# Performance work log

Hardware: AMD Instinct MI355X
Metric: run time of the kernel (lower is better)

## Reference

```python
import jax, jax.numpy as jnp
import numpy as np

B, D_IN, D_EXP, D_TOW, N_EXP, N_TASK = 16384, 1024, 1024, 512, 8, 4


def setup_inputs() -> dict:
    key = jax.random.key(0)
    ks = jax.random.split(key, 8)
    s_in = 1.0 / np.sqrt(D_IN)
    s_exp = 1.0 / np.sqrt(D_EXP)
    s_tow = 1.0 / np.sqrt(D_TOW)
    return {
        "x": jax.random.normal(ks[0], (B, D_IN), jnp.float32),
        # gate: ParameterList of num_experts vectors of size input_size -> [D_IN, N_EXP] matrix
        "gate_w": jax.random.normal(ks[1], (D_IN, N_EXP), jnp.float32) * s_in,
        # per-expert SLP: Linear(input_size, expert_size) + ReLU
        "exp_w": jax.random.normal(ks[2], (N_EXP, D_IN, D_EXP), jnp.float32) * s_in,
        "exp_b": jax.random.normal(ks[3], (N_EXP, D_EXP), jnp.float32) * 0.01,
        # per-task tower MLP: Linear(expert_size, tower_size) + ReLU + Linear(tower_size, 1)
        "tw1": jax.random.normal(ks[4], (N_TASK, D_EXP, D_TOW), jnp.float32) * s_exp,
        "tb1": jax.random.normal(ks[5], (N_TASK, D_TOW), jnp.float32) * 0.01,
        "tw2": jax.random.normal(ks[6], (N_TASK, D_TOW, 1), jnp.float32) * s_tow,
        "tb2": jax.random.normal(ks[7], (N_TASK, 1), jnp.float32) * 0.01,
    }


def reference(x, gate_w, exp_w, exp_b, tw1, tb1, tw2, tb2):
    # gates = x @ gate (no softmax in original)        [B, E]
    gates = x @ gate_w
    # all experts in one batched GEMM                  [E, B, D_exp]
    h = jax.nn.relu(jnp.einsum("bi,eid->ebd", x, exp_w) + exp_b[:, None, :])
    # fused gate-weighted combine (replaces the nested Python loops)
    shared = jnp.einsum("be,ebd->bd", gates, h)        # [B, D_exp]
    # per-task towers, batched over tasks
    t = jax.nn.relu(jnp.einsum("bd,tdh->tbh", shared, tw1) + tb1[:, None, :])
    outs = jnp.einsum("tbh,tho->tbo", t, tw2) + tb2[:, None, :]  # [T, B, 1]
    return outs
```

## Files before the change

### kernel.cpp

```cpp
#include <hip/hip_runtime.h>
#include <hip/hip_bf16.h>

#define B_DIM   16384
#define D_IN    1024
#define D_EXP   1024
#define D_TOW   512
#define N_EXPT  8
#define N_TASK  4

typedef _Float16 f16x8 __attribute__((ext_vector_type(8)));
typedef _Float16 f16x4 __attribute__((ext_vector_type(4)));
typedef float    f32x4 __attribute__((ext_vector_type(4)));

__device__ __forceinline__ void gll16(const void* g, void* l) {
  __builtin_amdgcn_global_load_lds(
      (const __attribute__((address_space(1))) unsigned int*)g,
      (__attribute__((address_space(3))) unsigned int*)l,
      16, 0, 0);
}

__device__ __forceinline__ f16x8 ldfrag(const _Float16* sM, int rowbase, int ks, int lane) {
  int rl = rowbase + (lane & 15);
  int ch = ((ks << 2) + (lane >> 4)) ^ (rl & 7);
  return *(const f16x8*)&sM[rl * 64 + ch * 8];
}

#define FENCE asm volatile("" ::: "memory")

__global__ __launch_bounds__(256) void prep_x_kernel(
    const float* __restrict__ x, const float* __restrict__ gw,
    _Float16* __restrict__ xh, float* __restrict__ gates)
{
  __shared__ float sred[4][8];
  const int t = threadIdx.x;
  const long row = blockIdx.x;
  float4 v = ((const float4*)(x + row * D_IN))[t];
  f16x4 h;
  h[0] = (_Float16)v.x; h[1] = (_Float16)v.y; h[2] = (_Float16)v.z; h[3] = (_Float16)v.w;
  ((f16x4*)(xh + row * D_IN))[t] = h;

  float g[8];
#pragma unroll
  for (int e = 0; e < 8; ++e) g[e] = 0.f;
  const float* wp = gw + (size_t)t * 4 * 8;
  float xs[4] = {v.x, v.y, v.z, v.w};
#pragma unroll
  for (int j = 0; j < 4; ++j)
#pragma unroll
    for (int e = 0; e < 8; ++e) g[e] += xs[j] * wp[j * 8 + e];

#pragma unroll
  for (int e = 0; e < 8; ++e) {
    g[e] += __shfl_xor(g[e], 1);  g[e] += __shfl_xor(g[e], 2);
    g[e] += __shfl_xor(g[e], 4);  g[e] += __shfl_xor(g[e], 8);
    g[e] += __shfl_xor(g[e], 16); g[e] += __shfl_xor(g[e], 32);
  }
  if ((t & 63) == 0) {
#pragma unroll
    for (int e = 0; e < 8; ++e) sred[t >> 6][e] = g[e];
  }
  __syncthreads();
  if (t < 8) gates[row * 8 + t] = sred[0][t] + sred[1][t] + sred[2][t] + sred[3][t];
}

__global__ __launch_bounds__(256) void transpose_cvt_kernel(
    const float* __restrict__ in, _Float16* __restrict__ outp, int K, int N)
{
  __shared__ float tile[64][65];
  const int t = threadIdx.x;
  const int tx = t & 63, ty = t >> 6;
  const int n0 = blockIdx.x * 64;
  const int k0 = blockIdx.y * 64;
  const long s = blockIdx.z;
  const float* ip = in + s * (long)K * N;
  _Float16* op = outp + s * (long)K * N;
#pragma unroll
  for (int i = 0; i < 16; ++i) {
    int r = ty * 16 + i;
    tile[r][tx] = ip[(long)(k0 + r) * N + n0 + tx];
  }
  __syncthreads();
#pragma unroll
  for (int i = 0; i < 16; ++i) {
    int r = ty * 16 + i;
    op[(long)(n0 + r) * K + k0 + tx] = (_Float16)tile[tx][r];
  }
}

__global__ void init_out_kernel(float* __restrict__ out, const float* __restrict__ tb2) {
  int i = blockIdx.x * 256 + threadIdx.x;
  if (i < N_TASK * B_DIM) out[i] = tb2[i >> 14];
}


#define LD_AF                                                                  \
    _Pragma("unroll") for (int mf = 0; mf < 4; ++mf)                           \
      _Pragma("unroll") for (int ks = 0; ks < 2; ++ks)                         \
        af[mf][ks] = ldfrag(sA, (wm & 1) * 64 + mf * 16, ks, lane)

#define LD_BF(SB)                                                              \
    _Pragma("unroll") for (int nf = 0; nf < 4; ++nf)                           \
      _Pragma("unroll") for (int ks = 0; ks < 2; ++ks)                         \
        bf[nf][ks] = ldfrag(SB, nf * 16, ks, lane)

#define MFMA32(ACC)                                                            \
    _Pragma("unroll") for (int mf = 0; mf < 4; ++mf)                           \
      _Pragma("unroll") for (int nf = 0; nf < 4; ++nf)                         \
        _Pragma("unroll") for (int ks = 0; ks < 2; ++ks)                       \
          ACC[mf][nf] = __builtin_amdgcn_mfma_f32_16x16x32_f16(                \
              af[mf][ks], bf[nf][ks], ACC[mf][nf], 0, 0, 0)

#define DRAIN_MFMA(ACC)                                                        \
    asm volatile("s_waitcnt lgkmcnt(0)" ::: "memory");                         \
    __builtin_amdgcn_sched_barrier(0);                                         \
    __builtin_amdgcn_s_setprio(1);                                             \
    MFMA32(ACC);                                                               \
    __builtin_amdgcn_s_setprio(0)

__global__ __launch_bounds__(512, 2) void moe_expert_kernel(
    const _Float16* __restrict__ xh,
    const _Float16* __restrict__ ewT,
    const float* __restrict__ expb,
    const float* __restrict__ gates,
    _Float16* __restrict__ shout)
{
  __shared__ alignas(16) _Float16 sT2[2][32768];
  __shared__ float sG[256 * 8];
  __shared__ _Float16 sBiasH[8 * 128];
  const int t = threadIdx.x;
  const int lane = t & 63;
  const int wave = t >> 6;
  const int wm = wave >> 1, wn = wave & 1;
  const long row0 = (long)blockIdx.x * 256;
  const int col0 = blockIdx.y * 128;

  for (int i = t; i < 256 * 8; i += 512) sG[i] = gates[row0 * 8 + i];
  for (int i = t; i < 8 * 128; i += 512)
    sBiasH[i] = (_Float16)expb[(i >> 7) * D_EXP + col0 + (i & 127)];

  const int so_t = (((t & 7) ^ ((t >> 3) & 7)) << 4);
  const char* aBase = (const char*)xh + row0 * 2048 + (size_t)(t >> 3) * 2048 + so_t;
  const char* bRoot = (const char*)ewT + (size_t)col0 * 2048 + (size_t)(t >> 3) * 2048 + so_t;

  auto SA = [&](int S, int kt) {
    const char* g = aBase + (size_t)(kt & 15) * 128;
    char* d = (char*)&sT2[S][0] + t * 16;
    gll16(g, d);            gll16(g + 131072, d + 8192);
    gll16(g + 262144, d + 16384); gll16(g + 393216, d + 24576);
    FENCE;
  };
  auto SB = [&](int S, int eloc, int e, int kt) {
    const char* g = bRoot + (size_t)e * 2097152 + (size_t)(kt & 15) * 128;
    char* d = (char*)&sT2[S][0] + 32768 + eloc * 16384 + t * 16;
    gll16(g, d); gll16(g + 131072, d + 8192);
    FENCE;
  };
  auto STAGE = [&](int S, int tau) {
    const int ep = tau >> 4, kt = tau & 15;
    SA(S, kt);
    SB(S, 0, 2 * ep, kt);
    SB(S, 1, 2 * ep + 1, kt);
  };

  __syncthreads();

  STAGE(0, 0);
  STAGE(1, 1);
  asm volatile("s_waitcnt vmcnt(8)" ::: "memory");
  __builtin_amdgcn_s_barrier();

  f32x4 acc0[4][4] = {};
  f32x4 acc1[4][4] = {};
  f16x4 shacc[4][4] = {};
  f16x8 af[4][2], bf[4][2];

#define TILE_E(CUR, TAU)                                                       \
  do {                                                                         \
    const int tau_ = (TAU);                                                    \
    const _Float16* sA  = &sT2[CUR][(wm >> 1) * 8192];                         \
    const _Float16* sB0 = &sT2[CUR][16384 + wn * 4096];                        \
    const _Float16* sB1 = &sT2[CUR][24576 + wn * 4096];                        \
    LD_AF; LD_BF(sB0);                                                         \
    DRAIN_MFMA(acc0);                                                          \
    LD_BF(sB1);                                                                \
    DRAIN_MFMA(acc1);                                                          \
    FENCE;                                                                     \
    __builtin_amdgcn_s_barrier();              \
    if (tau_ < 62) STAGE(CUR, tau_ + 2);                                       \
    if (tau_ < 62)      { asm volatile("s_waitcnt vmcnt(8)" ::: "memory"); }   \
    else if (tau_ == 62){ asm volatile("s_waitcnt vmcnt(0)" ::: "memory"); }   \
    if (tau_ < 63) __builtin_amdgcn_s_barrier();                               \
    if ((tau_ & 15) == 15) {                         \
      const int e0 = (tau_ >> 4) * 2;                                          \
      _Pragma("unroll") for (int ee = 0; ee < 2; ++ee) {                       \
        const int e = e0 + ee;                                                 \
        float bias4[4];                                                        \
        _Pragma("unroll") for (int nf = 0; nf < 4; ++nf)                       \
          bias4[nf] = (float)sBiasH[e * 128 + wn * 64 + nf * 16 + (lane & 15)];\
        _Pragma("unroll") for (int mf = 0; mf < 4; ++mf) {                     \
          int rbase = wm * 64 + mf * 16 + ((lane >> 4) << 2);                  \
          float gv[4];                                                         \
          _Pragma("unroll") for (int r = 0; r < 4; ++r)                        \
            gv[r] = sG[(rbase + r) * 8 + e];                                   \
          _Pragma("unroll") for (int nf = 0; nf < 4; ++nf) {                   \
            f16x4 sh = shacc[mf][nf];                                          \
            _Pragma("unroll") for (int r = 0; r < 4; ++r) {                    \
              float hv = (ee ? acc1[mf][nf][r] : acc0[mf][nf][r]) + bias4[nf]; \
              hv = hv > 0.f ? hv : 0.f;                                        \
              sh[r] += (_Float16)(gv[r] * hv);                                 \
              if (ee) acc1[mf][nf][r] = 0.f; else acc0[mf][nf][r] = 0.f;       \
            }                                                                  \
            shacc[mf][nf] = sh;                                                \
          }                                                                    \
        }                                                                      \
      }                                                                        \
    }                                                                          \
  } while (0)

  for (int tb = 0; tb < 64; tb += 2) {
    TILE_E(0, tb);
    TILE_E(1, tb + 1);
  }
#undef TILE_E

#pragma unroll
  for (int mf = 0; mf < 4; ++mf)
#pragma unroll
    for (int r = 0; r < 4; ++r) {
      long row = row0 + wm * 64 + mf * 16 + ((lane >> 4) << 2) + r;
      _Float16* op = shout + row * D_EXP + col0 + wn * 64 + (lane & 15);
#pragma unroll
      for (int nf = 0; nf < 4; ++nf) op[nf * 16] = shacc[mf][nf][r];
    }
}

__global__ __launch_bounds__(512, 2) void moe_tower_kernel(
    const _Float16* __restrict__ sh,
    const _Float16* __restrict__ t1T,
    const float* __restrict__ tb1,
    const float* __restrict__ tw2,
    float* __restrict__ out)
{
  __shared__ alignas(16) _Float16 sT2[2][32768];
  const int t = threadIdx.x;
  const int lane = t & 63;
  const int wave = t >> 6;
  const int wm = wave >> 1, wn = wave & 1;
  const long row0 = (long)blockIdx.x * 256;
  const int tp = blockIdx.y >> 2;
  const int col0 = (blockIdx.y & 3) * 128;

  float b1[2][4], w2[2][4];
#pragma unroll
  for (int ee = 0; ee < 2; ++ee)
#pragma unroll
    for (int nf = 0; nf < 4; ++nf) {
      int col = col0 + wn * 64 + nf * 16 + (lane & 15);
      b1[ee][nf] = tb1[(2 * tp + ee) * D_TOW + col];
      w2[ee][nf] = tw2[(2 * tp + ee) * D_TOW + col];
    }
  asm volatile("s_waitcnt vmcnt(0)" ::: "memory");

  const int so_t = (((t & 7) ^ ((t >> 3) & 7)) << 4);
  const char* aBase = (const char*)sh + row0 * 2048 + (size_t)(t >> 3) * 2048 + so_t;
  const char* bRoot = (const char*)t1T + (size_t)col0 * 2048
                      + (size_t)(t >> 3) * 2048 + so_t;

  auto SA = [&](int S, int kt) {
    const char* g = aBase + (size_t)kt * 128;
    char* d = (char*)&sT2[S][0] + t * 16;
    gll16(g, d);            gll16(g + 131072, d + 8192);
    gll16(g + 262144, d + 16384); gll16(g + 393216, d + 24576);
    FENCE;
  };
  auto SB = [&](int S, int eloc, int task, int kt) {
    const char* g = bRoot + (size_t)task * 1048576 + (size_t)kt * 128;
    char* d = (char*)&sT2[S][0] + 32768 + eloc * 16384 + t * 16;
    gll16(g, d); gll16(g + 131072, d + 8192);
    FENCE;
  };
  auto STAGE = [&](int S, int kt) {
    SA(S, kt);
    SB(S, 0, 2 * tp, kt);
    SB(S, 1, 2 * tp + 1, kt);
  };

  __syncthreads();

  STAGE(0, 0);
  STAGE(1, 1);
  asm volatile("s_waitcnt vmcnt(8)" ::: "memory");
  __builtin_amdgcn_s_barrier();

  f32x4 acc0[4][4] = {};
  f32x4 acc1[4][4] = {};
  f16x8 af[4][2], bf[4][2];

#define TILE_T(CUR, TAU)                                                       \
  do {                                                                         \
    const int tau_ = (TAU);                                                    \
    const _Float16* sA  = &sT2[CUR][(wm >> 1) * 8192];                         \
    const _Float16* sB0 = &sT2[CUR][16384 + wn * 4096];                        \
    const _Float16* sB1 = &sT2[CUR][24576 + wn * 4096];                        \
    LD_AF; LD_BF(sB0);                                                         \
    DRAIN_MFMA(acc0);                                                          \
    LD_BF(sB1);                                                                \
    DRAIN_MFMA(acc1);                                                          \
    FENCE;                                                                     \
    __builtin_amdgcn_s_barrier();                                              \
    if (tau_ < 14) STAGE(CUR, tau_ + 2);                                       \
    if (tau_ < 14)      { asm volatile("s_waitcnt vmcnt(8)" ::: "memory"); }   \
    else if (tau_ == 14){ asm volatile("s_waitcnt vmcnt(0)" ::: "memory"); }   \
    if (tau_ < 15) __builtin_amdgcn_s_barrier();                               \
  } while (0)

  for (int tb = 0; tb < 16; tb += 2) {
    TILE_T(0, tb);
    TILE_T(1, tb + 1);
  }
#undef TILE_T

#pragma unroll
  for (int mf = 0; mf < 4; ++mf)
#pragma unroll
    for (int r = 0; r < 4; ++r) {
#pragma unroll
      for (int ee = 0; ee < 2; ++ee) {
        float ssum = 0.f;
#pragma unroll
        for (int nf = 0; nf < 4; ++nf) {
          float v = (ee ? acc1[mf][nf][r] : acc0[mf][nf][r]) + b1[ee][nf];
          v = v > 0.f ? v : 0.f;
          ssum += v * w2[ee][nf];
        }
        ssum += __shfl_xor(ssum, 1);
        ssum += __shfl_xor(ssum, 2);
        ssum += __shfl_xor(ssum, 4);
        ssum += __shfl_xor(ssum, 8);
        if ((lane & 15) == 0) {
          long row = row0 + wm * 64 + mf * 16 + ((lane >> 4) << 2) + r;
          atomicAdd(&out[(size_t)(2 * tp + ee) * B_DIM + row], ssum);
        }
      }
    }
}

extern "C" void kernel_launch(void* const* d_in, const int* in_sizes, int n_in,
                              void* d_out, int out_size, void* d_ws, size_t ws_size,
                              hipStream_t stream) {
  const float* x    = (const float*)d_in[0];
  const float* gw   = (const float*)d_in[1];
  const float* expw = (const float*)d_in[2];
  const float* expb = (const float*)d_in[3];
  const float* tw1  = (const float*)d_in[4];
  const float* tb1  = (const float*)d_in[5];
  const float* tw2  = (const float*)d_in[6];
  const float* tb2  = (const float*)d_in[7];
  float* out = (float*)d_out;

  char* ws = (char*)d_ws;
  _Float16* xh  = (_Float16*)ws;  ws += (size_t)B_DIM * D_IN * 2;
  _Float16* ewT = (_Float16*)ws;  ws += (size_t)N_EXPT * D_IN * D_EXP * 2;
  _Float16* t1T = (_Float16*)ws;  ws += (size_t)N_TASK * D_TOW * D_EXP * 2;
  _Float16* shh = (_Float16*)ws;  ws += (size_t)B_DIM * D_EXP * 2;
  float* gates  = (float*)ws;     ws += (size_t)B_DIM * N_EXPT * 4;

  prep_x_kernel<<<B_DIM, 256, 0, stream>>>(x, gw, xh, gates);
  transpose_cvt_kernel<<<dim3(D_EXP / 64, D_IN / 64, N_EXPT), 256, 0, stream>>>(
      expw, ewT, D_IN, D_EXP);
  transpose_cvt_kernel<<<dim3(D_TOW / 64, D_EXP / 64, N_TASK), 256, 0, stream>>>(
      tw1, t1T, D_EXP, D_TOW);
  init_out_kernel<<<(N_TASK * B_DIM + 255) / 256, 256, 0, stream>>>(out, tb2);
  moe_expert_kernel<<<dim3(B_DIM / 256, D_EXP / 128), 512, 0, stream>>>(
      xh, ewT, expb, gates, shh);
  moe_tower_kernel<<<dim3(B_DIM / 256, (N_TASK * D_TOW) / 128), 512, 0, stream>>>(
      shh, t1T, tb1, tw2, out);
}
```

Baseline: 463.6 us.

## Shrink GEMM blocks to 128 rows with single LDS buffer and in-loop prefetch

Both GEMM kernels move from 512-thread, 256-row blocks with double-buffered LDS to 256-thread, 128-row blocks with a single 48KB LDS buffer. The next K-tile's global-to-LDS load is now issued after the first MFMA half and a barrier, and overlaps the second MFMA half. The smaller LDS footprint allows more blocks per CU and doubles the grid. In exchange, each tile of B is reused by fewer rows, and there is a full vmcnt(0) wait plus barrier every iteration.

```diff
diff --git a/kernel.cpp b/kernel.cpp
--- a/kernel.cpp
+++ b/kernel.cpp
@@ -96,7 +96,7 @@
 #define LD_AF                                                                  \
     _Pragma("unroll") for (int mf = 0; mf < 4; ++mf)                           \
       _Pragma("unroll") for (int ks = 0; ks < 2; ++ks)                         \
-        af[mf][ks] = ldfrag(sA, (wm & 1) * 64 + mf * 16, ks, lane)
+        af[mf][ks] = ldfrag(sA, mf * 16, ks, lane)
 
 #define LD_BF(SB)                                                              \
     _Pragma("unroll") for (int nf = 0; nf < 4; ++nf)                           \
@@ -110,118 +110,121 @@
           ACC[mf][nf] = __builtin_amdgcn_mfma_f32_16x16x32_f16(                \
               af[mf][ks], bf[nf][ks], ACC[mf][nf], 0, 0, 0)
 
-#define DRAIN_MFMA(ACC)                                                        \
-    asm volatile("s_waitcnt lgkmcnt(0)" ::: "memory");                         \
-    __builtin_amdgcn_sched_barrier(0);                                         \
-    __builtin_amdgcn_s_setprio(1);                                             \
-    MFMA32(ACC);                                                               \
-    __builtin_amdgcn_s_setprio(0)
-
-__global__ __launch_bounds__(512, 2) void moe_expert_kernel(
+__global__ __launch_bounds__(256, 2) void moe_expert_kernel(
     const _Float16* __restrict__ xh,
     const _Float16* __restrict__ ewT,
     const float* __restrict__ expb,
     const float* __restrict__ gates,
     _Float16* __restrict__ shout)
 {
-  __shared__ alignas(16) _Float16 sT2[2][32768];
-  __shared__ float sG[256 * 8];
+  __shared__ alignas(16) _Float16 sT[24576];
+  __shared__ float sG[128 * 8];
   __shared__ _Float16 sBiasH[8 * 128];
   const int t = threadIdx.x;
   const int lane = t & 63;
   const int wave = t >> 6;
   const int wm = wave >> 1, wn = wave & 1;
-  const long row0 = (long)blockIdx.x * 256;
+  const long row0 = (long)blockIdx.x * 128;
   const int col0 = blockIdx.y * 128;
 
-  for (int i = t; i < 256 * 8; i += 512) sG[i] = gates[row0 * 8 + i];
-  for (int i = t; i < 8 * 128; i += 512)
+  for (int i = t; i < 128 * 8; i += 256) sG[i] = gates[row0 * 8 + i];
+  for (int i = t; i < 8 * 128; i += 256)
     sBiasH[i] = (_Float16)expb[(i >> 7) * D_EXP + col0 + (i & 127)];
 
   const int so_t = (((t & 7) ^ ((t >> 3) & 7)) << 4);
   const char* aBase = (const char*)xh + row0 * 2048 + (size_t)(t >> 3) * 2048 + so_t;
   const char* bRoot = (const char*)ewT + (size_t)col0 * 2048 + (size_t)(t >> 3) * 2048 + so_t;
 
-  auto SA = [&](int S, int kt) {
+  auto SA = [&](int kt) {
     const char* g = aBase + (size_t)(kt & 15) * 128;
-    char* d = (char*)&sT2[S][0] + t * 16;
-    gll16(g, d);            gll16(g + 131072, d + 8192);
-    gll16(g + 262144, d + 16384); gll16(g + 393216, d + 24576);
-    FENCE;
-  };
-  auto SB = [&](int S, int eloc, int e, int kt) {
+    char* d = (char*)&sT[0] + t * 16;
+    gll16(g, d);                 gll16(g + 65536, d + 4096);
+    gll16(g + 131072, d + 8192); gll16(g + 196608, d + 12288);
+    FENCE;
+  };
+  auto SB = [&](int eloc, int e, int kt) {
     const char* g = bRoot + (size_t)e * 2097152 + (size_t)(kt & 15) * 128;
-    char* d = (char*)&sT2[S][0] + 32768 + eloc * 16384 + t * 16;
-    gll16(g, d); gll16(g + 131072, d + 8192);
-    FENCE;
-  };
-  auto STAGE = [&](int S, int tau) {
+    char* d = (char*)&sT[0] + 16384 + eloc * 16384 + t * 16;
+    gll16(g, d);                 gll16(g + 65536, d + 4096);
+    gll16(g + 131072, d + 8192); gll16(g + 196608, d + 12288);
+    FENCE;
+  };
+  auto STAGE = [&](int tau) {
     const int ep = tau >> 4, kt = tau & 15;
-    SA(S, kt);
-    SB(S, 0, 2 * ep, kt);
-    SB(S, 1, 2 * ep + 1, kt);
+    SA(kt);
+    SB(0, 2 * ep, kt);
+    SB(1, 2 * ep + 1, kt);
   };
 
   __syncthreads();
 
-  STAGE(0, 0);
-  STAGE(1, 1);
-  asm volatile("s_waitcnt vmcnt(8)" ::: "memory");
+  STAGE(0);
+  asm volatile("s_waitcnt vmcnt(0)" ::: "memory");
   __builtin_amdgcn_s_barrier();
+  FENCE;
 
   f32x4 acc0[4][4] = {};
   f32x4 acc1[4][4] = {};
   f16x4 shacc[4][4] = {};
   f16x8 af[4][2], bf[4][2];
 
-#define TILE_E(CUR, TAU)                                                       \
-  do {                                                                         \
-    const int tau_ = (TAU);                                                    \
-    const _Float16* sA  = &sT2[CUR][(wm >> 1) * 8192];                         \
-    const _Float16* sB0 = &sT2[CUR][16384 + wn * 4096];                        \
-    const _Float16* sB1 = &sT2[CUR][24576 + wn * 4096];                        \
-    LD_AF; LD_BF(sB0);                                                         \
-    DRAIN_MFMA(acc0);                                                          \
-    LD_BF(sB1);                                                                \
-    DRAIN_MFMA(acc1);                                                          \
-    FENCE;                                                                     \
-    __builtin_amdgcn_s_barrier();              \
-    if (tau_ < 62) STAGE(CUR, tau_ + 2);                                       \
-    if (tau_ < 62)      { asm volatile("s_waitcnt vmcnt(8)" ::: "memory"); }   \
-    else if (tau_ == 62){ asm volatile("s_waitcnt vmcnt(0)" ::: "memory"); }   \
-    if (tau_ < 63) __builtin_amdgcn_s_barrier();                               \
-    if ((tau_ & 15) == 15) {                         \
-      const int e0 = (tau_ >> 4) * 2;                                          \
-      _Pragma("unroll") for (int ee = 0; ee < 2; ++ee) {                       \
-        const int e = e0 + ee;                                                 \
-        float bias4[4];                                                        \
-        _Pragma("unroll") for (int nf = 0; nf < 4; ++nf)                       \
-          bias4[nf] = (float)sBiasH[e * 128 + wn * 64 + nf * 16 + (lane & 15)];\
-        _Pragma("unroll") for (int mf = 0; mf < 4; ++mf) {                     \
-          int rbase = wm * 64 + mf * 16 + ((lane >> 4) << 2);                  \
-          float gv[4];                                                         \
-          _Pragma("unroll") for (int r = 0; r < 4; ++r)                        \
-            gv[r] = sG[(rbase + r) * 8 + e];                                   \
-          _Pragma("unroll") for (int nf = 0; nf < 4; ++nf) {                   \
-            f16x4 sh = shacc[mf][nf];                                          \
-            _Pragma("unroll") for (int r = 0; r < 4; ++r) {                    \
-              float hv = (ee ? acc1[mf][nf][r] : acc0[mf][nf][r]) + bias4[nf]; \
-              hv = hv > 0.f ? hv : 0.f;                                        \
-              sh[r] += (_Float16)(gv[r] * hv);                                 \
-              if (ee) acc1[mf][nf][r] = 0.f; else acc0[mf][nf][r] = 0.f;       \
-            }                                                                  \
-            shacc[mf][nf] = sh;                                                \
-          }                                                                    \
-        }                                                                      \
-      }                                                                        \
-    }                                                                          \
-  } while (0)
-
-  for (int tb = 0; tb < 64; tb += 2) {
-    TILE_E(0, tb);
-    TILE_E(1, tb + 1);
-  }
-#undef TILE_E
+  const _Float16* sA  = &sT[wm * 4096];
+  const _Float16* sB0 = &sT[8192 + wn * 4096];
+  const _Float16* sB1 = &sT[16384 + wn * 4096];
+
+  for (int tau = 0; tau < 64; ++tau) {
+    LD_AF; LD_BF(sB0);
+    __builtin_amdgcn_s_setprio(1);
+    MFMA32(acc0);
+    __builtin_amdgcn_s_setprio(0);
+    LD_BF(sB1);
+    asm volatile("s_waitcnt lgkmcnt(0)" ::: "memory");
+    __builtin_amdgcn_sched_barrier(0);
+    FENCE;
+    __builtin_amdgcn_s_barrier();
+    FENCE;
+    if (tau < 63) STAGE(tau + 1);
+    __builtin_amdgcn_s_setprio(1);
+    MFMA32(acc1);
+    __builtin_amdgcn_s_setprio(0);
+    FENCE;
+    if (tau < 63) {
+      asm volatile("s_waitcnt vmcnt(0)" ::: "memory");
+      __builtin_amdgcn_s_barrier();
+      FENCE;
+    }
+
+    if ((tau & 15) == 15) {
+      const int e0 = (tau >> 4) * 2;
+#pragma unroll
+      for (int ee = 0; ee < 2; ++ee) {
+        const int e = e0 + ee;
+        float bias4[4];
+#pragma unroll
+        for (int nf = 0; nf < 4; ++nf)
+          bias4[nf] = (float)sBiasH[e * 128 + wn * 64 + nf * 16 + (lane & 15)];
+#pragma unroll
+        for (int mf = 0; mf < 4; ++mf) {
+          int rbase = wm * 64 + mf * 16 + ((lane >> 4) << 2);
+          float gv[4];
+#pragma unroll
+          for (int r = 0; r < 4; ++r) gv[r] = sG[(rbase + r) * 8 + e];
+#pragma unroll
+          for (int nf = 0; nf < 4; ++nf) {
+            f16x4 sh = shacc[mf][nf];
+#pragma unroll
+            for (int r = 0; r < 4; ++r) {
+              float hv = (ee ? acc1[mf][nf][r] : acc0[mf][nf][r]) + bias4[nf];
+              hv = hv > 0.f ? hv : 0.f;
+              sh[r] += (_Float16)(gv[r] * hv);
+              if (ee) acc1[mf][nf][r] = 0.f; else acc0[mf][nf][r] = 0.f;
+            }
+            shacc[mf][nf] = sh;
+          }
+        }
+      }
+    }
+  }
 
 #pragma unroll
   for (int mf = 0; mf < 4; ++mf)
@@ -234,19 +237,19 @@
     }
 }
 
-__global__ __launch_bounds__(512, 2) void moe_tower_kernel(
+__global__ __launch_bounds__(256, 2) void moe_tower_kernel(
     const _Float16* __restrict__ sh,
     const _Float16* __restrict__ t1T,
     const float* __restrict__ tb1,
     const float* __restrict__ tw2,
     float* __restrict__ out)
 {
-  __shared__ alignas(16) _Float16 sT2[2][32768];
+  __shared__ alignas(16) _Float16 sT[24576];
   const int t = threadIdx.x;
   const int lane = t & 63;
   const int wave = t >> 6;
   const int wm = wave >> 1, wn = wave & 1;
-  const long row0 = (long)blockIdx.x * 256;
+  const long row0 = (long)blockIdx.x * 128;
   const int tp = blockIdx.y >> 2;
   const int col0 = (blockIdx.y & 3) * 128;
 
@@ -266,59 +269,63 @@
   const char* bRoot = (const char*)t1T + (size_t)col0 * 2048
                       + (size_t)(t >> 3) * 2048 + so_t;
 
-  auto SA = [&](int S, int kt) {
+  auto SA = [&](int kt) {
     const char* g = aBase + (size_t)kt * 128;
-    char* d = (char*)&sT2[S][0] + t * 16;
-    gll16(g, d);            gll16(g + 131072, d + 8192);
-    gll16(g + 262144, d + 16384); gll16(g + 393216, d + 24576);
-    FENCE;
-  };
-  auto SB = [&](int S, int eloc, int task, int kt) {
+    char* d = (char*)&sT[0] + t * 16;
+    gll16(g, d);                 gll16(g + 65536, d + 4096);
+    gll16(g + 131072, d + 8192); gll16(g + 196608, d + 12288);
+    FENCE;
+  };
+  auto SB = [&](int eloc, int task, int kt) {
     const char* g = bRoot + (size_t)task * 1048576 + (size_t)kt * 128;
-    char* d = (char*)&sT2[S][0] + 32768 + eloc * 16384 + t * 16;
-    gll16(g, d); gll16(g + 131072, d + 8192);
-    FENCE;
-  };
-  auto STAGE = [&](int S, int kt) {
-    SA(S, kt);
-    SB(S, 0, 2 * tp, kt);
-    SB(S, 1, 2 * tp + 1, kt);
+    char* d = (char*)&sT[0] + 16384 + eloc * 16384 + t * 16;
+    gll16(g, d);                 gll16(g + 65536, d + 4096);
+    gll16(g + 131072, d + 8192); gll16(g + 196608, d + 12288);
+    FENCE;
+  };
+  auto STAGE = [&](int kt) {
+    SA(kt);
+    SB(0, 2 * tp, kt);
+    SB(1, 2 * tp + 1, kt);
   };
 
   __syncthreads();
 
-  STAGE(0, 0);
-  STAGE(1, 1);
-  asm volatile("s_waitcnt vmcnt(8)" ::: "memory");
+  STAGE(0);
+  asm volatile("s_waitcnt vmcnt(0)" ::: "memory");
   __builtin_amdgcn_s_barrier();
+  FENCE;
 
   f32x4 acc0[4][4] = {};
   f32x4 acc1[4][4] = {};
   f16x8 af[4][2], bf[4][2];
 
-#define TILE_T(CUR, TAU)                                                       \
-  do {                                                                         \
-    const int tau_ = (TAU);                                                    \
-    const _Float16* sA  = &sT2[CUR][(wm >> 1) * 8192];                         \
-    const _Float16* sB0 = &sT2[CUR][16384 + wn * 4096];                        \
-    const _Float16* sB1 = &sT2[CUR][24576 + wn * 4096];                        \
-    LD_AF; LD_BF(sB0);                                                         \
-    DRAIN_MFMA(acc0);                                                          \
-    LD_BF(sB1);                                                                \
-    DRAIN_MFMA(acc1);                                                          \
-    FENCE;                                                                     \
-    __builtin_amdgcn_s_barrier();                                              \
-    if (tau_ < 14) STAGE(CUR, tau_ + 2);                                       \
-    if (tau_ < 14)      { asm volatile("s_waitcnt vmcnt(8)" ::: "memory"); }   \
-    else if (tau_ == 14){ asm volatile("s_waitcnt vmcnt(0)" ::: "memory"); }   \
-    if (tau_ < 15) __builtin_amdgcn_s_barrier();                               \
-  } while (0)
-
-  for (int tb = 0; tb < 16; tb += 2) {
-    TILE_T(0, tb);
-    TILE_T(1, tb + 1);
-  }
-#undef TILE_T
+  const _Float16* sA  = &sT[wm * 4096];
+  const _Float16* sB0 = &sT[8192 + wn * 4096];
+  const _Float16* sB1 = &sT[16384 + wn * 4096];
+
+  for (int kt = 0; kt < 16; ++kt) {
+    LD_AF; LD_BF(sB0);
+    __builtin_amdgcn_s_setprio(1);
+    MFMA32(acc0);
+    __builtin_amdgcn_s_setprio(0);
+    LD_BF(sB1);
+    asm volatile("s_waitcnt lgkmcnt(0)" ::: "memory");
+    __builtin_amdgcn_sched_barrier(0);
+    FENCE;
+    __builtin_amdgcn_s_barrier();
+    FENCE;
+    if (kt < 15) STAGE(kt + 1);
+    __builtin_amdgcn_s_setprio(1);
+    MFMA32(acc1);
+    __builtin_amdgcn_s_setprio(0);
+    FENCE;
+    if (kt < 15) {
+      asm volatile("s_waitcnt vmcnt(0)" ::: "memory");
+      __builtin_amdgcn_s_barrier();
+      FENCE;
+    }
+  }
 
 #pragma unroll
   for (int mf = 0; mf < 4; ++mf)
@@ -371,8 +378,8 @@
   transpose_cvt_kernel<<<dim3(D_TOW / 64, D_EXP / 64, N_TASK), 256, 0, stream>>>(
       tw1, t1T, D_EXP, D_TOW);
   init_out_kernel<<<(N_TASK * B_DIM + 255) / 256, 256, 0, stream>>>(out, tb2);
-  moe_expert_kernel<<<dim3(B_DIM / 256, D_EXP / 128), 512, 0, stream>>>(
+  moe_expert_kernel<<<dim3(B_DIM / 128, D_EXP / 128), 256, 0, stream>>>(
       xh, ewT, expb, gates, shh);
-  moe_tower_kernel<<<dim3(B_DIM / 256, (N_TASK * D_TOW) / 128), 512, 0, stream>>>(
+  moe_tower_kernel<<<dim3(B_DIM / 128, 8), 256, 0, stream>>>(
       shh, t1T, tb1, tw2, out);
 }
```

New measurement: 399.0 us. 1.16x faster.
